# Kernel optimization log

Hardware: AMD Instinct MI355X
Metric: run time of the kernel (lower is better)

Reference implementation:

```python
import jax, jax.numpy as jnp
import numpy as np

N, E, D, H = 10000, 50000, 32, 4
DH = D // H  # head dim = 8


def setup_inputs() -> dict:
    key = jax.random.key(0)
    ks = jax.random.split(key, 16)
    f = lambda k, s: jax.random.normal(k, s, dtype=jnp.float32) * 0.1
    return {
        "in_feat":   f(ks[0], (N, D)),
        "query":     f(ks[1], (N, H, DH)),
        "src_key_w": f(ks[2], (E, H, DH, D)),
        "dst_key_w": f(ks[3], (E, H, DH, D)),
        "src_key_b": f(ks[4], (E, H, DH)),
        "dst_key_b": f(ks[5], (E, H, DH)),
        "src_val_w": f(ks[6], (E, H, DH, D)),
        "dst_val_w": f(ks[7], (E, H, DH, D)),
        "src_val_b": f(ks[8], (E, H, DH)),
        "dst_val_b": f(ks[9], (E, H, DH)),
        "node_w":    f(ks[10], (N, D, D)),
        "node_b":    f(ks[11], (N, D)),
        "ln_g":      jnp.ones((D,), jnp.float32),
        "ln_b":      jnp.zeros((D,), jnp.float32),
        "src":       jax.random.randint(ks[14], (E,), 0, N),
        "dst":       jax.random.randint(ks[15], (E,), 0, N),
    }


def _layer_norm(x, g, b, eps=1e-5):
    mu = jnp.mean(x, axis=-1, keepdims=True)
    var = jnp.var(x, axis=-1, keepdims=True)
    return (x - mu) * jax.lax.rsqrt(var + eps) * g + b


def reference(in_feat, query, src_key_w, dst_key_w, src_key_b, dst_key_b,
              src_val_w, dst_val_w, src_val_b, dst_val_b,
              node_w, node_b, ln_g, ln_b, src, dst):
    u = in_feat[src]  # [E, D] gathered src features
    v = in_feat[dst]  # [E, D] gathered dst features
    # edgewise_linear: per-edge weights, K = Wuk@u + buk + Wvk@v + bvk
    K = (jnp.einsum('ehdi,ei->ehd', src_key_w, u) + src_key_b
         + jnp.einsum('ehdi,ei->ehd', dst_key_w, v) + dst_key_b)  # [E,H,DH]
    V = (jnp.einsum('ehdi,ei->ehd', src_val_w, u) + src_val_b
         + jnp.einsum('ehdi,ei->ehd', dst_val_w, v) + dst_val_b)  # [E,H,DH]
    # e_dot_v(KEY, QUERY): score per edge against dst-node query
    score = jnp.einsum('ehd,ehd->eh', K, query[dst])  # [E, H]
    # edge_softmax: segment softmax over edges grouped by dst node
    smax = jax.ops.segment_max(score, dst, num_segments=N)  # [N, H]
    ex = jnp.exp(score - smax[dst])
    ssum = jax.ops.segment_sum(ex, dst, num_segments=N)
    attn = ex / ssum[dst]  # [E, H]
    # weighted values, scatter-sum to dst nodes
    feat = V * attn[..., None]  # [E, H, DH]
    agg = jax.ops.segment_sum(feat, dst, num_segments=N).reshape(N, D)
    # nodewise_linear with per-node weight, then relu
    out = jnp.einsum('noi,ni->no', node_w, agg) + node_b
    out = jax.nn.relu(out)
    out = in_feat + out              # residual
    out = _layer_norm(out, ln_g, ln_b)  # final LayerNorm
    return out, K.reshape(E, D), V.reshape(E, D), attn
```

## Files before the change

kernel.cpp:

```cpp
#include <hip/hip_runtime.h>
#include <hip/hip_bf16.h>
#include <math.h>

#define DD 32
#define HH 4

__device__ __forceinline__ void atomicMaxFloat(float* addr, float val) {
    if (val >= 0.0f) {
        atomicMax((int*)addr, __float_as_int(val));
    } else {
        atomicMin((unsigned int*)addr, __float_as_uint(val));
    }
}

__global__ __launch_bounds__(256) void edge_kernel(
    const float* __restrict__ in_feat,
    const float* __restrict__ query,
    const float* __restrict__ skw, const float* __restrict__ dkw,
    const float* __restrict__ skb, const float* __restrict__ dkb,
    const float* __restrict__ svw, const float* __restrict__ dvw,
    const float* __restrict__ svb, const float* __restrict__ dvb,
    const int* __restrict__ src, const int* __restrict__ dst,
    float* __restrict__ Kout,
    float* __restrict__ Vout,
    float* __restrict__ score,
    int E)
{
    const int e = blockIdx.x;
    if (e >= E) return;
    const int tid = threadIdx.x;
    const int r = tid >> 3;
    const int t = tid & 7;

    const int s = src[e];
    const int d = dst[e];

    const float4 u4 = *(const float4*)(in_feat + (size_t)s * DD + t * 4);
    const float4 v4 = *(const float4*)(in_feat + (size_t)d * DD + t * 4);

    const size_t woff = (size_t)e * 1024 + (size_t)r * 32 + (size_t)t * 4;

    float4 a = *(const float4*)(skw + woff);
    float4 b = *(const float4*)(dkw + woff);
    float pk = a.x * u4.x + a.y * u4.y + a.z * u4.z + a.w * u4.w
             + b.x * v4.x + b.y * v4.y + b.z * v4.z + b.w * v4.w;

    float4 c = *(const float4*)(svw + woff);
    float4 g = *(const float4*)(dvw + woff);
    float pv = c.x * u4.x + c.y * u4.y + c.z * u4.z + c.w * u4.w
             + g.x * v4.x + g.y * v4.y + g.z * v4.z + g.w * v4.w;

    #pragma unroll
    for (int m = 1; m <= 4; m <<= 1) {
        pk += __shfl_xor(pk, m);
        pv += __shfl_xor(pv, m);
    }

    float kval = 0.0f, q = 0.0f;
    if (t == 0) {
        const size_t bo = (size_t)e * DD + r;
        kval = pk + skb[bo] + dkb[bo];
        float vval = pv + svb[bo] + dvb[bo];
        Kout[bo] = kval;
        Vout[bo] = vval;
        q = query[(size_t)d * DD + r];
    }
    float prod = kval * q;
    #pragma unroll
    for (int m = 8; m <= 32; m <<= 1) prod += __shfl_xor(prod, m);
    if ((tid & 63) == 0) {
        const int h = tid >> 6;
        score[(size_t)e * HH + h] = prod;
    }
}

__global__ void init_kernel(float* __restrict__ smax, float* __restrict__ ssum,
                            float* __restrict__ agg, int NH, int ND)
{
    const int i = blockIdx.x * blockDim.x + threadIdx.x;
    if (i < NH) {
        smax[i] = __int_as_float(0xff800000);
        ssum[i] = 0.0f;
    }
    if (i < ND) agg[i] = 0.0f;
}

__global__ void smax_kernel(const float* __restrict__ score,
                            const int* __restrict__ dst,
                            float* __restrict__ smax, int EH)
{
    const int i = blockIdx.x * blockDim.x + threadIdx.x;
    if (i >= EH) return;
    const int e = i >> 2, h = i & 3;
    atomicMaxFloat(&smax[(size_t)dst[e] * HH + h], score[i]);
}

__global__ void esum_kernel(const float* __restrict__ score,
                            const int* __restrict__ dst,
                            const float* __restrict__ smax,
                            float* __restrict__ ex, float* __restrict__ ssum,
                            int EH)
{
    const int i = blockIdx.x * blockDim.x + threadIdx.x;
    if (i >= EH) return;
    const int e = i >> 2, h = i & 3;
    const int d = dst[e];
    const float x = expf(score[i] - smax[(size_t)d * HH + h]);
    ex[i] = x;
    atomicAdd(&ssum[(size_t)d * HH + h], x);
}

__global__ void attn_agg_kernel(const float* __restrict__ ex,
                                const float* __restrict__ ssum,
                                const int* __restrict__ dst,
                                const float* __restrict__ V,
                                float* __restrict__ attn_out,
                                float* __restrict__ agg,
                                int ED)
{
    const int i = blockIdx.x * blockDim.x + threadIdx.x;
    if (i >= ED) return;
    const int e = i >> 5, c = i & 31, h = c >> 3;
    const int d = dst[e];
    const float a = ex[(size_t)e * HH + h] / ssum[(size_t)d * HH + h];
    if ((c & 7) == 0) attn_out[(size_t)e * HH + h] = a;
    atomicAdd(&agg[(size_t)d * DD + c], V[i] * a);
}

__global__ __launch_bounds__(256) void node_kernel(
    const float* __restrict__ in_feat,
    const float* __restrict__ node_w,
    const float* __restrict__ node_b,
    const float* __restrict__ agg,
    const float* __restrict__ ln_g, const float* __restrict__ ln_b,
    float* __restrict__ out, int N)
{
    __shared__ float ys[DD];
    const int n = blockIdx.x;
    if (n >= N) return;
    const int tid = threadIdx.x;
    const int r = tid >> 3, t = tid & 7;

    const float4 a4 = *(const float4*)(agg + (size_t)n * DD + t * 4);
    const float4 w4 = *(const float4*)(node_w + (size_t)n * 1024 + (size_t)r * 32 + t * 4);
    float p = w4.x * a4.x + w4.y * a4.y + w4.z * a4.z + w4.w * a4.w;
    #pragma unroll
    for (int m = 1; m <= 4; m <<= 1) p += __shfl_xor(p, m);
    if (t == 0) {
        float y = p + node_b[(size_t)n * DD + r];
        y = fmaxf(y, 0.0f) + in_feat[(size_t)n * DD + r];
        ys[r] = y;
    }
    __syncthreads();
    if (tid < 64) {
        const float y = (tid < DD) ? ys[tid] : 0.0f;
        float sum = y;
        #pragma unroll
        for (int m = 1; m <= 32; m <<= 1) sum += __shfl_xor(sum, m);
        const float mu = sum * (1.0f / DD);
        const float dy = (tid < DD) ? (y - mu) : 0.0f;
        float s2 = dy * dy;
        #pragma unroll
        for (int m = 1; m <= 32; m <<= 1) s2 += __shfl_xor(s2, m);
        const float var = s2 * (1.0f / DD);
        if (tid < DD) {
            out[(size_t)n * DD + tid] =
                dy * rsqrtf(var + 1e-5f) * ln_g[tid] + ln_b[tid];
        }
    }
}

extern "C" void kernel_launch(void* const* d_in, const int* in_sizes, int n_in,
                              void* d_out, int out_size, void* d_ws, size_t ws_size,
                              hipStream_t stream) {
    const float* in_feat = (const float*)d_in[0];
    const float* query   = (const float*)d_in[1];
    const float* skw     = (const float*)d_in[2];
    const float* dkw     = (const float*)d_in[3];
    const float* skb     = (const float*)d_in[4];
    const float* dkb     = (const float*)d_in[5];
    const float* svw     = (const float*)d_in[6];
    const float* dvw     = (const float*)d_in[7];
    const float* svb     = (const float*)d_in[8];
    const float* dvb     = (const float*)d_in[9];
    const float* node_w  = (const float*)d_in[10];
    const float* node_b  = (const float*)d_in[11];
    const float* ln_g    = (const float*)d_in[12];
    const float* ln_b    = (const float*)d_in[13];
    const int*   src     = (const int*)d_in[14];
    const int*   dst     = (const int*)d_in[15];

    const int N = in_sizes[0] / DD;
    const int E = in_sizes[14];
    const int NH = N * HH, ND = N * DD;
    const int EH = E * HH, ED = E * DD;

    float* out_node = (float*)d_out;
    float* Kout     = out_node + (size_t)N * DD;
    float* Vout     = Kout + (size_t)E * DD;
    float* attn_out = Vout + (size_t)E * DD;

    float* ws    = (float*)d_ws;
    float* score = ws;
    float* ex    = score + EH;
    float* smax  = ex + EH;
    float* ssum  = smax + NH;
    float* agg   = ssum + NH;

    edge_kernel<<<E, 256, 0, stream>>>(in_feat, query, skw, dkw, skb, dkb,
                                       svw, dvw, svb, dvb, src, dst,
                                       Kout, Vout, score, E);
    init_kernel<<<(ND + 255) / 256, 256, 0, stream>>>(smax, ssum, agg, NH, ND);
    smax_kernel<<<(EH + 255) / 256, 256, 0, stream>>>(score, dst, smax, EH);
    esum_kernel<<<(EH + 255) / 256, 256, 0, stream>>>(score, dst, smax, ex, ssum, EH);
    attn_agg_kernel<<<(ED + 255) / 256, 256, 0, stream>>>(ex, ssum, dst, Vout,
                                                          attn_out, agg, ED);
    node_kernel<<<N, 256, 0, stream>>>(in_feat, node_w, node_b, agg,
                                       ln_g, ln_b, out_node, N);
}
```

Baseline: 181.0 us.

## Batch 32 edges per block with prefetched weight streaming and fused segment-max

The edge kernel now handles 32 edges per block instead of one. It gathers the src and dst features into LDS and streams each of the four weight tensors through a two-deep register prefetch, so that more loads are in flight. The atomic segment-max is folded into the edge kernel's score computation, and the separate smax kernel is removed, which saves a launch and a reread of the scores. In exchange, the weights are read in four sequential passes with a shuffle reduction per edge, fewer blocks are launched, and the block needs extra LDS and syncthreads.

```diff
diff --git a/kernel.cpp b/kernel.cpp
--- a/kernel.cpp
+++ b/kernel.cpp
@@ -4,12 +4,44 @@
 
 #define DD 32
 #define HH 4
+#define S_EDGES 32
 
 __device__ __forceinline__ void atomicMaxFloat(float* addr, float val) {
     if (val >= 0.0f) {
         atomicMax((int*)addr, __float_as_int(val));
     } else {
         atomicMin((unsigned int*)addr, __float_as_uint(val));
+    }
+}
+
+__device__ __forceinline__ float dot4(float4 a, float4 b) {
+    return a.x * b.x + a.y * b.y + a.z * b.z + a.w * b.w;
+}
+
+template<bool FIRST>
+__device__ __forceinline__ void weight_pass(
+    const float* __restrict__ W, size_t e0, int nE,
+    const float* __restrict__ featLds,
+    float* __restrict__ acc,
+    int tid)
+{
+    const int r = tid >> 3, t = tid & 7;
+    const float* gbase = W + e0 * 1024 + tid * 4;
+    float4 w0 = *(const float4*)(gbase);
+    float4 w1 = (nE > 1) ? *(const float4*)(gbase + 1024) : w0;
+    for (int j = 0; j < nE; ++j) {
+        const int jp = (j + 2 < nE) ? (j + 2) : (nE - 1);
+        const float4 w2 = *(const float4*)(gbase + (size_t)jp * 1024);
+        const float4 f = *(const float4*)(featLds + j * 32 + t * 4);
+        float p = dot4(w0, f);
+        p += __shfl_xor(p, 1);
+        p += __shfl_xor(p, 2);
+        p += __shfl_xor(p, 4);
+        if (t == 0) {
+            if (FIRST) acc[j * 32 + r] = p;
+            else       acc[j * 32 + r] += p;
+        }
+        w0 = w1; w1 = w2;
     }
 }
 
@@ -24,53 +56,75 @@
     float* __restrict__ Kout,
     float* __restrict__ Vout,
     float* __restrict__ score,
+    float* __restrict__ smax,
     int E)
 {
-    const int e = blockIdx.x;
-    if (e >= E) return;
+    __shared__ int   idx_s[S_EDGES], idx_d[S_EDGES];
+    __shared__ float uf[S_EDGES * DD];
+    __shared__ float vf[S_EDGES * DD];
+    __shared__ float acc[S_EDGES * DD];
+
     const int tid = threadIdx.x;
-    const int r = tid >> 3;
-    const int t = tid & 7;
-
-    const int s = src[e];
-    const int d = dst[e];
-
-    const float4 u4 = *(const float4*)(in_feat + (size_t)s * DD + t * 4);
-    const float4 v4 = *(const float4*)(in_feat + (size_t)d * DD + t * 4);
-
-    const size_t woff = (size_t)e * 1024 + (size_t)r * 32 + (size_t)t * 4;
-
-    float4 a = *(const float4*)(skw + woff);
-    float4 b = *(const float4*)(dkw + woff);
-    float pk = a.x * u4.x + a.y * u4.y + a.z * u4.z + a.w * u4.w
-             + b.x * v4.x + b.y * v4.y + b.z * v4.z + b.w * v4.w;
-
-    float4 c = *(const float4*)(svw + woff);
-    float4 g = *(const float4*)(dvw + woff);
-    float pv = c.x * u4.x + c.y * u4.y + c.z * u4.z + c.w * u4.w
-             + g.x * v4.x + g.y * v4.y + g.z * v4.z + g.w * v4.w;
+    const int e0i = blockIdx.x * S_EDGES;
+    if (e0i >= E) return;
+    const size_t e0 = (size_t)e0i;
+    const int nE = (E - e0i < S_EDGES) ? (E - e0i) : S_EDGES;
+
+    if (tid < S_EDGES) {
+        int ee = e0i + tid; if (ee >= E) ee = E - 1;
+        idx_s[tid] = src[ee];
+    } else if (tid < 2 * S_EDGES) {
+        int ee = e0i + tid - S_EDGES; if (ee >= E) ee = E - 1;
+        idx_d[tid - S_EDGES] = dst[ee];
+    }
+    __syncthreads();
+
+    {
+        const int j = tid >> 3, t = tid & 7;
+        *(float4*)(uf + j * 32 + t * 4) =
+            *(const float4*)(in_feat + (size_t)idx_s[j] * DD + t * 4);
+        *(float4*)(vf + j * 32 + t * 4) =
+            *(const float4*)(in_feat + (size_t)idx_d[j] * DD + t * 4);
+    }
+    __syncthreads();
+
+    weight_pass<true >(skw, e0, nE, uf, acc, tid);
+    weight_pass<false>(dkw, e0, nE, vf, acc, tid);
+    __syncthreads();
 
     #pragma unroll
-    for (int m = 1; m <= 4; m <<= 1) {
-        pk += __shfl_xor(pk, m);
-        pv += __shfl_xor(pv, m);
-    }
-
-    float kval = 0.0f, q = 0.0f;
-    if (t == 0) {
-        const size_t bo = (size_t)e * DD + r;
-        kval = pk + skb[bo] + dkb[bo];
-        float vval = pv + svb[bo] + dvb[bo];
-        Kout[bo] = kval;
-        Vout[bo] = vval;
-        q = query[(size_t)d * DD + r];
-    }
-    float prod = kval * q;
+    for (int i = 0; i < S_EDGES / 8; ++i) {
+        const int j = i * 8 + (tid >> 5);
+        const int r = tid & 31;
+        if (j < nE) {
+            const size_t e = e0 + j;
+            const float kv = acc[j * 32 + r] + skb[e * DD + r] + dkb[e * DD + r];
+            Kout[e * DD + r] = kv;
+            float p = kv * query[(size_t)idx_d[j] * DD + r];
+            p += __shfl_xor(p, 1);
+            p += __shfl_xor(p, 2);
+            p += __shfl_xor(p, 4);
+            if ((r & 7) == 0) {
+                const int h = r >> 3;
+                score[e * HH + h] = p;
+                atomicMaxFloat(&smax[(size_t)idx_d[j] * HH + h], p);
+            }
+        }
+    }
+    __syncthreads();
+
+    weight_pass<true >(svw, e0, nE, uf, acc, tid);
+    weight_pass<false>(dvw, e0, nE, vf, acc, tid);
+    __syncthreads();
+
     #pragma unroll
-    for (int m = 8; m <= 32; m <<= 1) prod += __shfl_xor(prod, m);
-    if ((tid & 63) == 0) {
-        const int h = tid >> 6;
-        score[(size_t)e * HH + h] = prod;
+    for (int i = 0; i < S_EDGES / 8; ++i) {
+        const int j = i * 8 + (tid >> 5);
+        const int r = tid & 31;
+        if (j < nE) {
+            const size_t e = e0 + j;
+            Vout[e * DD + r] = acc[j * 32 + r] + svb[e * DD + r] + dvb[e * DD + r];
+        }
     }
 }
 
@@ -83,16 +137,6 @@
         ssum[i] = 0.0f;
     }
     if (i < ND) agg[i] = 0.0f;
-}
-
-__global__ void smax_kernel(const float* __restrict__ score,
-                            const int* __restrict__ dst,
-                            float* __restrict__ smax, int EH)
-{
-    const int i = blockIdx.x * blockDim.x + threadIdx.x;
-    if (i >= EH) return;
-    const int e = i >> 2, h = i & 3;
-    atomicMaxFloat(&smax[(size_t)dst[e] * HH + h], score[i]);
 }
 
 __global__ void esum_kernel(const float* __restrict__ score,
@@ -207,11 +251,10 @@
     float* ssum  = smax + NH;
     float* agg   = ssum + NH;
 
-    edge_kernel<<<E, 256, 0, stream>>>(in_feat, query, skw, dkw, skb, dkb,
-                                       svw, dvw, svb, dvb, src, dst,
-                                       Kout, Vout, score, E);
     init_kernel<<<(ND + 255) / 256, 256, 0, stream>>>(smax, ssum, agg, NH, ND);
-    smax_kernel<<<(EH + 255) / 256, 256, 0, stream>>>(score, dst, smax, EH);
+    edge_kernel<<<(E + S_EDGES - 1) / S_EDGES, 256, 0, stream>>>(
+        in_feat, query, skw, dkw, skb, dkb, svw, dvw, svb, dvb, src, dst,
+        Kout, Vout, score, smax, E);
     esum_kernel<<<(EH + 255) / 256, 256, 0, stream>>>(score, dst, smax, ex, ssum, EH);
     attn_agg_kernel<<<(ED + 255) / 256, 256, 0, stream>>>(ex, ssum, dst, Vout,
                                                           attn_out, agg, ED);
```

After: 190.8 us. +5.4%, slower.
